# Kernel tuning notes

Hardware: AMD Instinct MI355X
Metric: run time of the kernel (lower is better)

The kernel has to match this reference:

```python
import jax, jax.numpy as jnp
import numpy as np
from jax import lax

D_MODEL = 200
N_LAYER = 12
NHEADS = 8
HEADDIM = 50
D_STATE = 64
D_INNER = 2 * D_MODEL            # 400
CONV_DIM = D_INNER + 2 * D_STATE  # 528 (ngroups=1)
D_IN_PROJ = 2 * D_INNER + 2 * D_STATE + NHEADS  # 936
D_CONV = 4
EPS = 1e-5


def rmsnorm(x, w):
    v = jnp.mean(jnp.square(x), axis=-1, keepdims=True)
    return x * lax.rsqrt(v + EPS) * w


def groupnorm(x, groups, g, b):
    B, C, H, W = x.shape
    xg = x.reshape(B, groups, C // groups, H, W)
    mu = jnp.mean(xg, axis=(2, 3, 4), keepdims=True)
    var = jnp.mean(jnp.square(xg - mu), axis=(2, 3, 4), keepdims=True)
    xn = ((xg - mu) * lax.rsqrt(var + EPS)).reshape(B, C, H, W)
    return xn * g[:, None, None] + b[:, None, None]


def patch_embed(x, pe_conv_w, proj_in_w, gn_g, gn_b, spec_w):
    b, c, l, d = x.shape
    # time path: 'b c l d' -> (b, 1, c*l, d), conv -> (b, 25, c*l, 8)
    time_x = x.reshape(b, 1, c * l, d)
    t = lax.conv_general_dilated(time_x, proj_in_w, (1, 25), ((0, 0), (24, 24)),
                                 dimension_numbers=('NCHW', 'OIHW', 'NCHW'))
    t = jax.nn.gelu(groupnorm(t, 5, gn_g, gn_b), approximate=False)
    time_emb = t.transpose(0, 2, 1, 3).reshape(b, c, l, D_MODEL)
    # freq path: rfft over patch dim, norm='forward'
    spec = jnp.abs(jnp.fft.rfft(x, axis=-1, norm='forward'))  # (b,c,l,101)
    spec_emb = jnp.einsum('bclf,df->bcld', spec, spec_w)
    patch = time_emb + spec_emb
    # depthwise 7x7 positional conv over (d, c, l)
    pos = lax.conv_general_dilated(patch.transpose(0, 3, 1, 2), pe_conv_w, (1, 1),
                                   ((3, 3), (3, 3)),
                                   dimension_numbers=('NCHW', 'OIHW', 'NCHW'),
                                   feature_group_count=D_MODEL)
    return patch + pos.transpose(0, 2, 3, 1)


def ssd_scan(xh, dt, B, C, A, D):
    # xh: (b,l,h,p)  dt: (b,l,h)  B,C: (b,l,n)  A,D: (h,)
    b, l, h, p = xh.shape

    def step(state, inp):
        x_t, dt_t, B_t, C_t = inp
        dA = jnp.exp(dt_t * A)  # (b,h)
        state = state * dA[:, :, None, None] + \
            (dt_t[:, :, None, None] * x_t[:, :, :, None]) * B_t[:, None, None, :]
        y = jnp.einsum('bhpn,bn->bhp', state, C_t)
        return state, y

    state0 = jnp.zeros((b, h, p, D_STATE), xh.dtype)
    _, ys = lax.scan(step, state0,
                     (xh.transpose(1, 0, 2, 3), dt.transpose(1, 0, 2),
                      B.transpose(1, 0, 2), C.transpose(1, 0, 2)))
    return ys.transpose(1, 0, 2, 3) + xh * D[None, None, :, None]


def mamba2(u, in_w, conv_w, conv_b, dt_bias, A_log, D, gn_w, out_w):
    b, l, _ = u.shape
    zxbcdt = u @ in_w.T  # (b,l,936)
    z = zxbcdt[..., :D_INNER]
    xBC = zxbcdt[..., D_INNER:D_INNER + CONV_DIM]
    dt = jax.nn.softplus(zxbcdt[..., D_INNER + CONV_DIM:] + dt_bias)  # (b,l,8)
    # causal depthwise conv1d, kernel 4
    xc = lax.conv_general_dilated(xBC.transpose(0, 2, 1), conv_w, (1,), ((D_CONV - 1, 0),),
                                  dimension_numbers=('NCH', 'OIH', 'NCH'),
                                  feature_group_count=CONV_DIM)
    xBC = jax.nn.silu((xc + conv_b[:, None]).transpose(0, 2, 1))
    x = xBC[..., :D_INNER].reshape(b, l, NHEADS, HEADDIM)
    Bm = xBC[..., D_INNER:D_INNER + D_STATE]
    Cm = xBC[..., D_INNER + D_STATE:]
    y = ssd_scan(x, dt, Bm, Cm, -jnp.exp(A_log), D).reshape(b, l, D_INNER)
    y = rmsnorm(y * jax.nn.silu(z), gn_w)  # RMSNormGated, norm_before_gate=False
    return y @ out_w.T


@jax.checkpoint
def layer(hidden, residual, norm_w, in_w, conv_w, conv_b, dt_bias, A_log, D, gn_w, out_w):
    residual = hidden + residual
    hidden = mamba2(rmsnorm(residual, norm_w), in_w, conv_w, conv_b, dt_bias, A_log, D, gn_w, out_w)
    return hidden, residual


def forward(x, pe_conv_w, proj_in_w, gn_g, gn_b, spec_w, norm_w, in_proj_w, conv_w, conv_b,
            dt_bias, A_log, D, gnorm_w, out_proj_w, norm_f_w, head_w, head_b):
    b, c, l, d = x.shape
    hidden = patch_embed(x, pe_conv_w, proj_in_w, gn_g, gn_b, spec_w).reshape(b, c * l, d)
    residual = jnp.zeros_like(hidden)
    for i in range(N_LAYER):
        hidden, residual = layer(hidden, residual, norm_w[i], in_proj_w[i], conv_w[i],
                                 conv_b[i], dt_bias[i], A_log[i], D[i], gnorm_w[i], out_proj_w[i])
    hidden = rmsnorm(hidden + residual, norm_f_w).reshape(b, c, l, d)
    return hidden @ head_w.T + head_b


def setup_inputs():
    key = jax.random.key(0)
    ks = jax.random.split(key, 12)
    B, CH, L, P = 16, 19, 30, 200

    def g(k, shape, scale):
        return jax.random.normal(k, shape, jnp.float32) * scale

    dt = jax.random.uniform(ks[8], (N_LAYER, NHEADS), jnp.float32, 1e-3, 0.1)
    return {
        'x': g(ks[0], (B, CH, L, P), 1.0),
        'pe_conv_w': g(ks[1], (D_MODEL, 1, 7, 7), 0.15),
        'proj_in_w': g(ks[2], (25, 1, 1, 49), 0.14),
        'gn_g': jnp.ones(25, jnp.float32),
        'gn_b': jnp.zeros(25, jnp.float32),
        'spec_w': g(ks[3], (D_MODEL, 101), 0.1),
        'norm_w': jnp.ones((N_LAYER, D_MODEL), jnp.float32),
        'in_proj_w': g(ks[4], (N_LAYER, D_IN_PROJ, D_MODEL), 0.07),
        'conv_w': g(ks[5], (N_LAYER, CONV_DIM, 1, D_CONV), 0.4),
        'conv_b': jnp.zeros((N_LAYER, CONV_DIM), jnp.float32),
        'dt_bias': jnp.log(jnp.expm1(dt)),
        'A_log': jnp.log(jax.random.uniform(ks[9], (N_LAYER, NHEADS), jnp.float32, 1.0, 16.0)),
        'D': jnp.ones((N_LAYER, NHEADS), jnp.float32),
        'gnorm_w': jnp.ones((N_LAYER, D_INNER), jnp.float32),
        'out_proj_w': g(ks[6], (N_LAYER, D_MODEL, D_INNER), 0.05),
        'norm_f_w': jnp.ones(D_MODEL, jnp.float32),
        'head_w': g(ks[7], (D_MODEL, D_MODEL), 0.07),
        'head_b': jnp.zeros(D_MODEL, jnp.float32),
    }


def reference(x, pe_conv_w, proj_in_w, gn_g, gn_b, spec_w, norm_w, in_proj_w, conv_w, conv_b,
              dt_bias, A_log, D, gnorm_w, out_proj_w, norm_f_w, head_w, head_b):
    return forward(x, pe_conv_w, proj_in_w, gn_g, gn_b, spec_w, norm_w, in_proj_w, conv_w,
                   conv_b, dt_bias, A_log, D, gnorm_w, out_proj_w, norm_f_w, head_w, head_b)
```

## Files before the change

kernel.cpp:

```cpp
#include <hip/hip_runtime.h>
#include <hip/hip_bf16.h>
#include <math.h>

#define D_MODEL   200
#define N_LAYER   12
#define NHEADS    8
#define HEADDIM   50
#define D_STATE   64
#define D_INNER   400
#define CONV_DIM  528
#define D_IN_PROJ 936
#define D_CONV    4
#define EPS       1e-5f

#define BATCH 16
#define CH    19
#define LLEN  30
#define SEQ   570
#define NTOK  9120
#define NFREQ 101

typedef __attribute__((ext_vector_type(8))) short s8v;
typedef __attribute__((ext_vector_type(4))) float f32x4;

// ... 416 lines not shown
        dtb[(size_t)m * NHEADS + h] = (raw > 20.f) ? raw : log1pf(expf(raw));
    }
}

__global__ __launch_bounds__(256) void dt_gemv_kernel(
    const float* __restrict__ u, const float* __restrict__ Win,
    const float* __restrict__ dt_bias, float* __restrict__ dtb, int layer)
{
    int tid = threadIdx.x;
    int tok = blockIdx.x * 4 + (tid >> 6);
    int head = (tid >> 3) & 7;
    int l8 = tid & 7;
    const float* ur = u + (size_t)tok * 200;
    const float* wr = Win + (size_t)layer * D_IN_PROJ * 200 + (size_t)(928 + head) * 200;
    float s = 0.f;
    for (int k = l8; k < 200; k += 8) s = fmaf(ur[k], wr[k], s);
    s += __shfl_xor(s, 1, 64);
    s += __shfl_xor(s, 2, 64);
    s += __shfl_xor(s, 4, 64);
    if (l8 == 0) {
        float raw = s + dt_bias[layer * NHEADS + head];
        dtb[(size_t)tok * NHEADS + head] = (raw > 20.f) ? raw : log1pf(expf(raw));
    }
}

__global__ __launch_bounds__(256) void dtconv2_kernel(
    const float* __restrict__ zxbcdt, const float* __restrict__ cw,
    const float* __restrict__ cb, float* __restrict__ xBC, int layer)
{
    int b = blockIdx.x, tt = blockIdx.y;
    int t0 = tt * 8;
    __shared__ float zs[11][528];
    const float* cwl = cw + (size_t)layer * CONV_DIM * 4;
    const float* cbl = cb + (size_t)layer * CONV_DIM;
    for (int i = threadIdx.x; i < 11 * 528; i += 256) {
        int r = i / 528, ch = i - r * 528;
        int t = t0 - 3 + r;
        zs[r][ch] = (t >= 0 && t < SEQ)
                        ? zxbcdt[(size_t)(b * SEQ + t) * D_IN_PROJ + D_INNER + ch] : 0.f;
    }
    __syncthreads();
    for (int o = threadIdx.x; o < 8 * 528; o += 256) {
        int tr = o / 528, ch = o - tr * 528;
        int t = t0 + tr;
        if (t >= SEQ) continue;
        float acc = cbl[ch];
#pragma unroll
        for (int k = 0; k < 4; k++)
            acc = fmaf(zs[tr + k][ch], cwl[ch * 4 + k], acc);
        xBC[(size_t)(b * SEQ + t) * CONV_DIM + ch] = acc / (1.f + expf(-acc));
    }
}

__global__ __launch_bounds__(512) void ssd_state3_kernel(
    const float* __restrict__ xBC, const float* __restrict__ dtb,
    const float* __restrict__ A_log, float* __restrict__ Sbuf,
    float* __restrict__ Pd, int layer, int lchunk, int nchunk)
{
    int b = blockIdx.x, c = blockIdx.y;
    int tid = threadIdx.x;
    int h = tid >> 6, p = tid & 63;
    float A = -expf(A_log[layer * NHEADS + h]);

    __shared__ __align__(16) float sh[2][2][536];
    int t0 = c * lchunk;
    int npairs = lchunk >> 1, rem = lchunk & 1;

    {
        if (tid < 264) {
            int wch = (tid >= 132) ? 1 : 0;
            int fidx = tid - wch * 132;
            int tq = t0 + wch;
            float4 v = ((const float4*)(xBC + (size_t)(b * SEQ + tq) * CONV_DIM))[fidx];
            *(float4*)&sh[0][wch][fidx * 4] = v;
        } else if (tid < 280) {
            int e = tid - 264, tok = e >> 3, hd = e & 7;
            sh[0][tok][528 + hd] = dtb[(size_t)(b * SEQ + t0 + tok) * NHEADS + hd];
        }
    }
    __syncthreads();

    float s[64];
#pragma unroll
    for (int n = 0; n < 64; n++) s[n] = 0.f;
    float pacc = 1.f;

    for (int i = 0; i < npairs; i++) {
        int t = t0 + 2 * i;
        int buf = i & 1, nb = buf ^ 1;
        bool pf = (2 * i + 2 < lchunk);
        float4 rx;
        float rdt = 0.f;
        int wch = 0, fidx = 0;
        if (pf) {
            if (tid < 264) {
                wch = (tid >= 132) ? 1 : 0;
                fidx = tid - wch * 132;
                int tq = t + 2 + wch; if (tq > SEQ - 1) tq = SEQ - 1;
                rx = ((const float4*)(xBC + (size_t)(b * SEQ + tq) * CONV_DIM))[fidx];
            } else if (tid < 280) {
                int e = tid - 264, tok = e >> 3, hd = e & 7;
                int tq = t + 2 + tok; if (tq > SEQ - 1) tq = SEQ - 1;
                rdt = dtb[(size_t)(b * SEQ + tq) * NHEADS + hd];
            }
        }
#pragma unroll
        for (int k = 0; k < 2; k++) {
            float dtv = sh[buf][k][528 + h];
            float xp  = (p < HEADDIM) ? sh[buf][k][h * HEADDIM + p] : 0.f;
            float dA = __expf(dtv * A);
            float u  = dtv * xp;
            pacc *= dA;
            const float4* B4 = (const float4*)&sh[buf][k][D_INNER];
#pragma unroll
            for (int n4 = 0; n4 < 16; n4++) {
                float4 bq = B4[n4];
                s[4 * n4 + 0] = fmaf(s[4 * n4 + 0], dA, u * bq.x);
                s[4 * n4 + 1] = fmaf(s[4 * n4 + 1], dA, u * bq.y);
                s[4 * n4 + 2] = fmaf(s[4 * n4 + 2], dA, u * bq.z);
                s[4 * n4 + 3] = fmaf(s[4 * n4 + 3], dA, u * bq.w);
            }
        }
        if (pf) {
            if (tid < 264) *(float4*)&sh[nb][wch][fidx * 4] = rx;
            else if (tid < 280) { int e = tid - 264; sh[nb][e >> 3][528 + (e & 7)] = rdt; }
        }
        __syncthreads();
    }

    if (rem) {
        int buf = npairs & 1;
        float dtv = sh[buf][0][528 + h];
        float xp  = (p < HEADDIM) ? sh[buf][0][h * HEADDIM + p] : 0.f;
        float dA = __expf(dtv * A);
        float u  = dtv * xp;
        pacc *= dA;
        const float4* B4 = (const float4*)&sh[buf][0][D_INNER];
#pragma unroll
        for (int n4 = 0; n4 < 16; n4++) {
            float4 bq = B4[n4];
            s[4 * n4 + 0] = fmaf(s[4 * n4 + 0], dA, u * bq.x);
            s[4 * n4 + 1] = fmaf(s[4 * n4 + 1], dA, u * bq.y);
            s[4 * n4 + 2] = fmaf(s[4 * n4 + 2], dA, u * bq.z);
            s[4 * n4 + 3] = fmaf(s[4 * n4 + 3], dA, u * bq.w);
        }
    }

    if (p < HEADDIM) {
        float* Sb = Sbuf + ((size_t)((b * NHEADS + h) * nchunk + c)) * (HEADDIM * 64)
                    + p * 64;
#pragma unroll
        for (int n4 = 0; n4 < 16; n4++)
            ((float4*)Sb)[n4] = make_float4(s[4 * n4], s[4 * n4 + 1],
                                            s[4 * n4 + 2], s[4 * n4 + 3]);
    }
    if (p == 0) Pd[(b * NHEADS + h) * nchunk + c] = pacc;
}

__global__ __launch_bounds__(512) void ssd_state_kernel(
    const float* __restrict__ xBC, const float* __restrict__ dtb,
    const float* __restrict__ A_log, float* __restrict__ Sbuf,
    float* __restrict__ Pd, int layer, int lchunk, int nchunk)
{
    int b = blockIdx.x, c = blockIdx.y;
    int tid = threadIdx.x;
    int h = tid >> 6, p = tid & 63;
    float A = -expf(A_log[layer * NHEADS + h]);

    __shared__ float sh[2][544];
    int t0 = c * lchunk, tend = t0 + lchunk;

    {
        const float* base = xBC + (size_t)(b * SEQ + t0) * CONV_DIM;
        sh[0][tid] = base[tid];
        if (tid < 24) {
            int e2 = 512 + tid;
            sh[0][e2] = (e2 < 528) ? base[e2]
                                   : dtb[(size_t)(b * SEQ + t0) * NHEADS + (e2 - 528)];
        }
    }
    __syncthreads();

    float s[64];
#pragma unroll
    for (int n = 0; n < 64; n++) s[n] = 0.f;
    float pacc = 1.f;

    for (int t = t0; t < tend; t++) {
        int cur = (t - t0) & 1, nxt = cur ^ 1;
        float pf0 = 0.f, pf1 = 0.f;
        if (t + 1 < tend) {
            const float* base = xBC + (size_t)(b * SEQ + t + 1) * CONV_DIM;
            pf0 = base[tid];
            if (tid < 24) {
                int e2 = 512 + tid;
                pf1 = (e2 < 528) ? base[e2]
                                 : dtb[(size_t)(b * SEQ + t + 1) * NHEADS + (e2 - 528)];
            }
        }
        float dtv = sh[cur][528 + h];
        float xp  = (p < HEADDIM) ? sh[cur][h * HEADDIM + p] : 0.f;
        float dA = __expf(dtv * A);
        float u  = dtv * xp;
        pacc *= dA;
        const float4* B4 = (const float4*)&sh[cur][D_INNER];
#pragma unroll
        for (int n4 = 0; n4 < 16; n4++) {
            float4 bq = B4[n4];
            s[4 * n4 + 0] = fmaf(s[4 * n4 + 0], dA, u * bq.x);
            s[4 * n4 + 1] = fmaf(s[4 * n4 + 1], dA, u * bq.y);
            s[4 * n4 + 2] = fmaf(s[4 * n4 + 2], dA, u * bq.z);
            s[4 * n4 + 3] = fmaf(s[4 * n4 + 3], dA, u * bq.w);
        }
        if (t + 1 < tend) {
            sh[nxt][tid] = pf0;
            if (tid < 24) sh[nxt][512 + tid] = pf1;
        }
        __syncthreads();
    }

    if (p < HEADDIM) {
        float* Sb = Sbuf + ((size_t)((b * NHEADS + h) * nchunk + c)) * (HEADDIM * 64)
                    + p * 64;
#pragma unroll
        for (int n4 = 0; n4 < 16; n4++)
            ((float4*)Sb)[n4] = make_float4(s[4 * n4], s[4 * n4 + 1],
                                            s[4 * n4 + 2], s[4 * n4 + 3]);
    }
    if (p == 0) Pd[(b * NHEADS + h) * nchunk + c] = pacc;
}

__global__ __launch_bounds__(256) void ssd_scan2b_kernel(
    float* __restrict__ Sbuf, const float* __restrict__ Pd, int nchunk)
{
    int bh = blockIdx.x;
    int e = blockIdx.y * 256 + threadIdx.x;
    if (e >= HEADDIM * 64) return;
    float* base = Sbuf + (size_t)bh * nchunk * (HEADDIM * 64) + e;
    const float* pd = Pd + bh * nchunk;
    float cur = 0.f;
    for (int c = 0; c < nchunk; c++) {
        float l = base[(size_t)c * (HEADDIM * 64)];
        base[(size_t)c * (HEADDIM * 64)] = cur;
        cur = fmaf(pd[c], cur, l);
    }
}

__global__ __launch_bounds__(512) void ssd_out_fused3_kernel(
    const float* __restrict__ xBC, const float* __restrict__ dtb,
    const float* __restrict__ zxbcdt, const float* __restrict__ A_log,
    const float* __restrict__ Dv, const float* __restrict__ Sbuf,
    const float* __restrict__ gw, short* __restrict__ ybf,
    int layer, int lchunk, int nchunk)
{
    int b = blockIdx.x, c = blockIdx.y;
    int tid = threadIdx.x;
    int h = tid >> 6, p = tid & 63;
    float A = -expf(A_log[layer * NHEADS + h]);
    float Dh = Dv[layer * NHEADS + h];
    float gval = (p < HEADDIM) ? gw[(size_t)layer * D_INNER + h * HEADDIM + p] : 0.f;

    __shared__ __align__(16) float sh[2][2][536];
    __shared__ __align__(16) float shz[2][2][400];
    __shared__ float red[2][2][8];
    int t0 = c * lchunk;
    int npairs = lchunk >> 1, rem = lchunk & 1;

    {
        if (tid < 264) {
            int wch = (tid >= 132) ? 1 : 0;
            int fidx = tid - wch * 132;
            int tq = t0 + wch;
            float4 v = ((const float4*)(xBC + (size_t)(b * SEQ + tq) * CONV_DIM))[fidx];
            *(float4*)&sh[0][wch][fidx * 4] = v;
        } else if (tid < 280) {
            int e = tid - 264, tok = e >> 3, hd = e & 7;
            sh[0][tok][528 + hd] = dtb[(size_t)(b * SEQ + t0 + tok) * NHEADS + hd];
        } else if (tid < 480) {
            int wch = (tid >= 380) ? 1 : 0;
            int fidx = tid - 280 - wch * 100;
            int tq = t0 + wch;
            float4 v = ((const float4*)(zxbcdt + (size_t)(b * SEQ + tq) * D_IN_PROJ))[fidx];
            *(float4*)&shz[0][wch][fidx * 4] = v;
        }
    }

    float s[64];
    if (p < HEADDIM) {
        const float* Sb = Sbuf + ((size_t)((b * NHEADS + h) * nchunk + c)) * (HEADDIM * 64)
                          + p * 64;
#pragma unroll
        for (int n4 = 0; n4 < 16; n4++) {
            float4 v = ((const float4*)Sb)[n4];
            s[4 * n4] = v.x; s[4 * n4 + 1] = v.y; s[4 * n4 + 2] = v.z; s[4 * n4 + 3] = v.w;
        }
    } else {
#pragma unroll
        for (int n = 0; n < 64; n++) s[n] = 0.f;
    }
    __syncthreads();

    for (int i = 0; i < npairs; i++) {
        int t = t0 + 2 * i;
        int buf = i & 1, nb = buf ^ 1;
        bool pf = (2 * i + 2 < lchunk);
        float4 rx, rz;
        float rdt = 0.f;
        int wch = 0, fidx = 0, zwch = 0, zfidx = 0;
        if (pf) {
            if (tid < 264) {
                wch = (tid >= 132) ? 1 : 0;
                fidx = tid - wch * 132;
                int tq = t + 2 + wch; if (tq > SEQ - 1) tq = SEQ - 1;
                rx = ((const float4*)(xBC + (size_t)(b * SEQ + tq) * CONV_DIM))[fidx];
            } else if (tid < 280) {
                int e = tid - 264, tok = e >> 3, hd = e & 7;
                int tq = t + 2 + tok; if (tq > SEQ - 1) tq = SEQ - 1;
                rdt = dtb[(size_t)(b * SEQ + tq) * NHEADS + hd];
            } else if (tid < 480) {
                zwch = (tid >= 380) ? 1 : 0;
                zfidx = tid - 280 - zwch * 100;
                int tq = t + 2 + zwch; if (tq > SEQ - 1) tq = SEQ - 1;
                rz = ((const float4*)(zxbcdt + (size_t)(b * SEQ + tq) * D_IN_PROJ))[zfidx];
            }
        }
        float g0 = 0.f, g1 = 0.f;
#pragma unroll
        for (int k = 0; k < 2; k++) {
            float dtv = sh[buf][k][528 + h];
            float xp  = (p < HEADDIM) ? sh[buf][k][h * HEADDIM + p] : 0.f;
            float dA = __expf(dtv * A);
            float u  = dtv * xp;
            const float4* B4 = (const float4*)&sh[buf][k][D_INNER];
            const float4* C4 = (const float4*)&sh[buf][k][D_INNER + D_STATE];
            float y0 = 0.f, y1 = 0.f, y2 = 0.f, y3 = 0.f;
#pragma unroll
            for (int n4 = 0; n4 < 16; n4++) {
                float4 bq = B4[n4];
                float4 cq = C4[n4];
                float t0v = fmaf(s[4 * n4 + 0], dA, u * bq.x);
                float t1v = fmaf(s[4 * n4 + 1], dA, u * bq.y);
                float t2v = fmaf(s[4 * n4 + 2], dA, u * bq.z);
                float t3v = fmaf(s[4 * n4 + 3], dA, u * bq.w);
                s[4 * n4 + 0] = t0v; s[4 * n4 + 1] = t1v;
                s[4 * n4 + 2] = t2v; s[4 * n4 + 3] = t3v;
                y0 = fmaf(t0v, cq.x, y0);
                y1 = fmaf(t1v, cq.y, y1);
                y2 = fmaf(t2v, cq.z, y2);
                y3 = fmaf(t3v, cq.w, y3);
            }
            if (p < HEADDIM) {
                float yv = fmaf(xp, Dh, (y0 + y1) + (y2 + y3));
                float zv = shz[buf][k][h * HEADDIM + p];
                float g = yv * (zv / (1.f + expf(-zv)));
                if (k == 0) g0 = g; else g1 = g;
            }
        }
        float gs0 = g0 * g0, gs1 = g1 * g1;
#pragma unroll
        for (int o = 32; o; o >>= 1) {
            gs0 += __shfl_xor(gs0, o, 64);
            gs1 += __shfl_xor(gs1, o, 64);
        }
        if (p == 0) { red[buf][0][h] = gs0; red[buf][1][h] = gs1; }
        if (pf) {
            if (tid < 264) *(float4*)&sh[nb][wch][fidx * 4] = rx;
            else if (tid < 280) { int e = tid - 264; sh[nb][e >> 3][528 + (e & 7)] = rdt; }
            else if (tid < 480) *(float4*)&shz[nb][zwch][zfidx * 4] = rz;
        }
        __syncthreads();
        float tot0 = (red[buf][0][0] + red[buf][0][1]) + (red[buf][0][2] + red[buf][0][3]) +
                     (red[buf][0][4] + red[buf][0][5]) + (red[buf][0][6] + red[buf][0][7]);
        float tot1 = (red[buf][1][0] + red[buf][1][1]) + (red[buf][1][2] + red[buf][1][3]) +
                     (red[buf][1][4] + red[buf][1][5]) + (red[buf][1][6] + red[buf][1][7]);
        float rstd0 = rsqrtf(tot0 * (1.f / D_INNER) + EPS);
        float rstd1 = rsqrtf(tot1 * (1.f / D_INNER) + EPS);
        size_t row0 = (size_t)(b * SEQ + t) * 416;
        size_t row1 = (size_t)(b * SEQ + t + 1) * 416;
        if (p < HEADDIM) {
            ybf[row0 + h * HEADDIM + p] = f2bf(g0 * rstd0 * gval);
            ybf[row1 + h * HEADDIM + p] = f2bf(g1 * rstd1 * gval);
        } else {
            int widx = h * 14 + (p - HEADDIM);
            if (widx < 16) {
                ybf[row0 + 400 + widx] = 0;
                ybf[row1 + 400 + widx] = 0;
            }
        }
    }

    if (rem) {
        int buf = npairs & 1;
        int t = t0 + lchunk - 1;
        float g0 = 0.f;
        {
            float dtv = sh[buf][0][528 + h];
            float xp  = (p < HEADDIM) ? sh[buf][0][h * HEADDIM + p] : 0.f;
            float dA = __expf(dtv * A);
            float u  = dtv * xp;
            const float4* B4 = (const float4*)&sh[buf][0][D_INNER];
            const float4* C4 = (const float4*)&sh[buf][0][D_INNER + D_STATE];
            float y0 = 0.f, y1 = 0.f, y2 = 0.f, y3 = 0.f;
#pragma unroll
            for (int n4 = 0; n4 < 16; n4++) {
                float4 bq = B4[n4];
                float4 cq = C4[n4];
                float t0v = fmaf(s[4 * n4 + 0], dA, u * bq.x);
                float t1v = fmaf(s[4 * n4 + 1], dA, u * bq.y);
                float t2v = fmaf(s[4 * n4 + 2], dA, u * bq.z);
                float t3v = fmaf(s[4 * n4 + 3], dA, u * bq.w);
                s[4 * n4 + 0] = t0v; s[4 * n4 + 1] = t1v;
                s[4 * n4 + 2] = t2v; s[4 * n4 + 3] = t3v;
                y0 = fmaf(t0v, cq.x, y0);
                y1 = fmaf(t1v, cq.y, y1);
                y2 = fmaf(t2v, cq.z, y2);
                y3 = fmaf(t3v, cq.w, y3);
            }
            if (p < HEADDIM) {
                float yv = fmaf(xp, Dh, (y0 + y1) + (y2 + y3));
                float zv = shz[buf][0][h * HEADDIM + p];
                g0 = yv * (zv / (1.f + expf(-zv)));
            }
        }
        float gs0 = g0 * g0;
#pragma unroll
        for (int o = 32; o; o >>= 1) gs0 += __shfl_xor(gs0, o, 64);
        if (p == 0) red[buf][0][h] = gs0;
        __syncthreads();
        float tot0 = (red[buf][0][0] + red[buf][0][1]) + (red[buf][0][2] + red[buf][0][3]) +
                     (red[buf][0][4] + red[buf][0][5]) + (red[buf][0][6] + red[buf][0][7]);
        float rstd0 = rsqrtf(tot0 * (1.f / D_INNER) + EPS);
        size_t row0 = (size_t)(b * SEQ + t) * 416;
        if (p < HEADDIM) {
            ybf[row0 + h * HEADDIM + p] = f2bf(g0 * rstd0 * gval);
        } else {
            int widx = h * 14 + (p - HEADDIM);
            if (widx < 16) ybf[row0 + 400 + widx] = 0;
        }
    }
}

__global__ __launch_bounds__(512) void ssd_out_kernel(
    const float* __restrict__ xBC, const float* __restrict__ dtb,
    const float* __restrict__ A_log, const float* __restrict__ Dv,
    const float* __restrict__ Sbuf, float* __restrict__ y,
    int layer, int lchunk, int nchunk)
{
    int b = blockIdx.x, c = blockIdx.y;
    int tid = threadIdx.x;
    int h = tid >> 6, p = tid & 63;
    float A = -expf(A_log[layer * NHEADS + h]);
    float Dh = Dv[layer * NHEADS + h];

    __shared__ float sh[2][544];
    int t0 = c * lchunk, tend = t0 + lchunk;

    {
        const float* base = xBC + (size_t)(b * SEQ + t0) * CONV_DIM;
        sh[0][tid] = base[tid];
        if (tid < 24) {
            int e2 = 512 + tid;
            sh[0][e2] = (e2 < 528) ? base[e2]
                                   : dtb[(size_t)(b * SEQ + t0) * NHEADS + (e2 - 528)];
        }
    }

    float s[64];
    if (p < HEADDIM) {
        const float* Sb = Sbuf + ((size_t)((b * NHEADS + h) * nchunk + c)) * (HEADDIM * 64)
                          + p * 64;
#pragma unroll
        for (int n4 = 0; n4 < 16; n4++) {
            float4 v = ((const float4*)Sb)[n4];
            s[4 * n4] = v.x; s[4 * n4 + 1] = v.y; s[4 * n4 + 2] = v.z; s[4 * n4 + 3] = v.w;
        }
    } else {
#pragma unroll
        for (int n = 0; n < 64; n++) s[n] = 0.f;
    }
    __syncthreads();

    for (int t = t0; t < tend; t++) {
        int cur = (t - t0) & 1, nxt = cur ^ 1;
        float pf0 = 0.f, pf1 = 0.f;
        if (t + 1 < tend) {
            const float* base = xBC + (size_t)(b * SEQ + t + 1) * CONV_DIM;
            pf0 = base[tid];
            if (tid < 24) {
                int e2 = 512 + tid;
                pf1 = (e2 < 528) ? base[e2]
// ... 45 lines not shown
    float* yr = y + (size_t)m * D_INNER;
    const float* gwl = gw + (size_t)layer * D_INNER;
    float ss = 0.f;
    for (int k = threadIdx.x; k < D_INNER; k += 256) {
        float zv = z[k];
        float sz = zv / (1.f + expf(-zv));
        float g = yr[k] * sz;
        buf[k] = g;
        ss = fmaf(g, g, ss);
    }
    int lane = threadIdx.x & 63, w = threadIdx.x >> 6;
#pragma unroll
    for (int o = 32; o; o >>= 1) ss += __shfl_xor(ss, o, 64);
    if (lane == 0) red[w] = ss;
    __syncthreads();
    float tot = red[0] + red[1] + red[2] + red[3];
    float rstd = rsqrtf(tot * (1.f / D_INNER) + EPS);
    for (int k = threadIdx.x; k < 416; k += 256) {
        if (k < D_INNER) {
            float v = buf[k] * rstd * gwl[k];
            yr[k] = v;
            if (ybf) ybf[(size_t)m * 416 + k] = f2bf(v);
        } else if (ybf) {
            ybf[(size_t)m * 416 + k] = 0;
        }
    }
}

extern "C" void kernel_launch(void* const* d_in, const int* in_sizes, int n_in,
                              void* d_out, int out_size, void* d_ws, size_t ws_size,
                              hipStream_t stream)
{
    const float* x         = (const float*)d_in[0];
    const float* pe_conv_w = (const float*)d_in[1];
    const float* proj_in_w = (const float*)d_in[2];
    const float* gn_g      = (const float*)d_in[3];
    const float* gn_b      = (const float*)d_in[4];
    const float* spec_w    = (const float*)d_in[5];
    const float* norm_w    = (const float*)d_in[6];
    const float* in_proj_w = (const float*)d_in[7];
    const float* conv_w    = (const float*)d_in[8];
    const float* conv_b    = (const float*)d_in[9];
    const float* dt_bias   = (const float*)d_in[10];
    const float* A_log     = (const float*)d_in[11];
    const float* Dv        = (const float*)d_in[12];
    const float* gnorm_w   = (const float*)d_in[13];
    const float* out_proj_w= (const float*)d_in[14];
    const float* norm_f_w  = (const float*)d_in[15];
    const float* head_w    = (const float*)d_in[16];
    const float* head_b    = (const float*)d_in[17];
    float* out = (float*)d_out;
    float* ws  = (float*)d_ws;

    const size_t needA = 27929344ull * sizeof(float);
    int fast = (ws_size >= needA) ? 1 : 0;

    int nchunk, lchunk;
    float *residual = ws, *hidden = ws + 1824000;
    float *zxbcdt, *xBC, *dtb, *Sbuf, *Pd;
    float *ubuf = nullptr, *ybuf = nullptr;
    short *w_in_bf = nullptr, *w_out_bf = nullptr, *w_head_bf = nullptr,
          *w_spec_bf = nullptr, *csmat_bf = nullptr, *x_bf = nullptr,
          *ubuf_bf = nullptr, *ybuf_bf = nullptr, *magb_bf = nullptr;

    if (fast) {
        nchunk = 15; lchunk = 38;
        zxbcdt = ws + 3648000;
        xBC    = ws + 12184320;
        dtb    = ws + 16999680;
        Sbuf   = ws + 17072640;
        Pd     = ws + 23216640;
        short* pool = (short*)(ws + 23218560);
        w_in_bf   = pool;
        w_out_bf  = pool + 2515968;
        w_head_bf = pool + 3514368;
        w_spec_bf = pool + 3559168;
        ubuf_bf   = pool + 3584768;
        ybuf_bf   = pool + 5627648;
        csmat_bf  = (short*)(Sbuf + 4000000);
        x_bf      = (short*)(Sbuf + 4100000);
        magb_bf   = (short*)(Sbuf + 5200000);
    } else {
        nchunk = 6; lchunk = 95;
        ubuf   = ws + 3648000;
        zxbcdt = ws + 5472000;
        xBC    = ws + 14008320;
        dtb    = ws + 18823680;
        ybuf   = ws + 18896640;
        Sbuf   = ws + 1824000;
        Pd     = ws + 5470000;
    }

    float* traw  = fast ? Sbuf : ybuf;
    float* patch = zxbcdt;
    float* csout = fast ? (Sbuf + 2000000) : (xBC + 50000);
    float* csmat = xBC;
    float* magb  = fast ? nullptr : (xBC + 2000000);
    float* stats = dtb;

    if (fast) {
        cast_pad_kernel<<<(12 * 936 * 224 + 255) / 256, 256, 0, stream>>>(
            in_proj_w, w_in_bf, 12 * 936, 200, 224);
        cast_pad_kernel<<<(12 * 200 * 416 + 255) / 256, 256, 0, stream>>>(
            out_proj_w, w_out_bf, 12 * 200, 400, 416);
        cast_pad_kernel<<<(200 * 224 + 255) / 256, 256, 0, stream>>>(
            head_w, w_head_bf, 200, 200, 224);
        cast_pad_kernel<<<(200 * 128 + 255) / 256, 256, 0, stream>>>(
            spec_w, w_spec_bf, 200, 101, 128);
        cast_pad_kernel<<<(9120 * 224 + 255) / 256, 256, 0, stream>>>(
            x, x_bf, 9120, 200, 224);
        dft_init_bf_kernel<<<(202 * 224 + 255) / 256, 256, 0, stream>>>(csmat_bf);
    } else {
        dft_init_kernel<<<(202 * 200 + 255) / 256, 256, 0, stream>>>(csmat);
    }

    time_conv_kernel<<<NTOK, 256, 0, stream>>>(x, proj_in_w, traw);
    gn_stats_kernel<<<80, 256, 0, stream>>>(traw, stats);
    gn_gelu_kernel<<<(NTOK * 200 + 255) / 256, 256, 0, stream>>>(traw, stats, gn_g, gn_b, patch);
    if (fast) {
        gemm_bf16<<<dim3(2, 72), 256, 0, stream>>>(x_bf, csmat_bf, nullptr, csout,
                                                   NTOK, 202, 224, 0);
        mag_bf_kernel<<<(NTOK * 128 + 255) / 256, 256, 0, stream>>>(csout, magb_bf);
        gemm_bf16<<<dim3(2, 72), 256, 0, stream>>>(magb_bf, w_spec_bf, nullptr, patch,
                                                   NTOK, 200, 128, 1);
    } else {
        gemm_nt<<<dim3(2, 72), 256, 0, stream>>>(x, csmat, nullptr, csout, NTOK, 202, 200, 0);
        mag_kernel<<<(NTOK * NFREQ + 255) / 256, 256, 0, stream>>>(csout, magb);
        gemm_nt<<<dim3(2, 72), 256, 0, stream>>>(magb, spec_w, nullptr, patch,
                                                 NTOK, 200, NFREQ, 1);
    }
    pe_conv3_kernel<<<dim3(16, 13, 5), 256, 0, stream>>>(patch, pe_conv_w, hidden);

    for (int i = 0; i < N_LAYER; i++) {
        if (fast) {
            norm_dt_kernel<<<NTOK, 256, 0, stream>>>(hidden, residual, norm_w + i * 200,
                                                     ubuf_bf, in_proj_w, dt_bias, dtb,
                                                     i, (i == 0) ? 1 : 0);
            gemm_bf16<<<dim3(8, 72), 256, 0, stream>>>(
                ubuf_bf, w_in_bf + (size_t)i * 936 * 224, nullptr, zxbcdt,
                NTOK, D_IN_PROJ, 224, 0);
        } else {
            add_rmsnorm_kernel<<<NTOK, 64, 0, stream>>>(hidden, residual, norm_w + i * 200,
                                                        ubuf, nullptr, (i == 0) ? 1 : 0);
            dt_gemv_kernel<<<NTOK / 4, 256, 0, stream>>>(ubuf, in_proj_w, dt_bias, dtb, i);
            gemm_nt<<<dim3(8, 72), 256, 0, stream>>>(
                ubuf, in_proj_w + (size_t)i * D_IN_PROJ * 200, nullptr, zxbcdt,
                NTOK, D_IN_PROJ, 200, 0);
        }
        dtconv2_kernel<<<dim3(16, 72), 256, 0, stream>>>(zxbcdt, conv_w, conv_b, xBC, i);
        {
            dim3 g(BATCH, nchunk);
            if (fast) {
                ssd_state3_kernel<<<g, 512, 0, stream>>>(xBC, dtb, A_log, Sbuf, Pd,
                                                         i, lchunk, nchunk);
                ssd_scan2b_kernel<<<dim3(BATCH * NHEADS, 13), 256, 0, stream>>>(Sbuf, Pd, nchunk);
                ssd_out_fused3_kernel<<<g, 512, 0, stream>>>(
                    xBC, dtb, zxbcdt, A_log, Dv, Sbuf, gnorm_w, ybuf_bf, i, lchunk, nchunk);
                gemm_bf16<<<dim3(2, 72), 256, 0, stream>>>(
                    ybuf_bf, w_out_bf + (size_t)i * 200 * 416, nullptr, hidden,
                    NTOK, 200, 416, 0);
            } else {
                ssd_state_kernel<<<g, 512, 0, stream>>>(xBC, dtb, A_log, Sbuf, Pd,
                                                        i, lchunk, nchunk);
                ssd_scan2b_kernel<<<dim3(BATCH * NHEADS, 13), 256, 0, stream>>>(Sbuf, Pd, nchunk);
                ssd_out_kernel<<<g, 512, 0, stream>>>(xBC, dtb, A_log, Dv, Sbuf, ybuf,
                                                      i, lchunk, nchunk);
                gate_norm_kernel<<<NTOK, 256, 0, stream>>>(ybuf, zxbcdt, gnorm_w, nullptr, i);
                gemm_nt<<<dim3(2, 72), 256, 0, stream>>>(
                    ybuf, out_proj_w + (size_t)i * 200 * D_INNER, nullptr, hidden,
                    NTOK, 200, D_INNER, 0);
            }
        }
    }

    add_rmsnorm_kernel<<<NTOK, 64, 0, stream>>>(hidden, residual, norm_f_w,
                                                fast ? nullptr : ubuf,
                                                fast ? ubuf_bf : nullptr, 0);
    if (fast) {
        gemm_bf16<<<dim3(2, 72), 256, 0, stream>>>(ubuf_bf, w_head_bf, head_b, out,
                                                   NTOK, 200, 224, 0);
    } else {
        gemm_nt<<<dim3(2, 72), 256, 0, stream>>>(ubuf, head_w, head_b, out,
                                                 NTOK, 200, 200, 0);
    }
}
```

Baseline: 2.542 ms.

## Compute local chunk outputs in state pass; apply inter-chunk correction separately

The first scan kernel now produces each token's within-chunk output (including the D skip term) and the running decay product, in addition to the chunk-final states. It uses a triple-buffered shared-memory prefetch that loads two token pairs ahead. A new correction kernel adds the carried-in state contribution, scaled by the prefix decay, as a C·S0 dot product, then applies the gate and RMS norm. This removes the second full recurrence over B that the old output kernel redid. In exchange it writes and reads an extra fp32 y buffer and prefix array in a larger workspace. The odd-length remainder path was dropped, so the code assumes lchunk is even (38 here).

```diff
diff --git a/kernel.cpp b/kernel.cpp
--- a/kernel.cpp
+++ b/kernel.cpp
@@ -492,30 +492,33 @@
     }
 }
 
-__global__ __launch_bounds__(512) void ssd_state3_kernel(
+__global__ __launch_bounds__(512) void ssd_scanA_kernel(
     const float* __restrict__ xBC, const float* __restrict__ dtb,
-    const float* __restrict__ A_log, float* __restrict__ Sbuf,
-    float* __restrict__ Pd, int layer, int lchunk, int nchunk)
+    const float* __restrict__ A_log, const float* __restrict__ Dv,
+    float* __restrict__ ylocal, float* __restrict__ Pref,
+    float* __restrict__ Sbuf, float* __restrict__ Pd,
+    int layer, int lchunk, int nchunk)
 {
     int b = blockIdx.x, c = blockIdx.y;
     int tid = threadIdx.x;
     int h = tid >> 6, p = tid & 63;
     float A = -expf(A_log[layer * NHEADS + h]);
-
-    __shared__ __align__(16) float sh[2][2][536];
+    float Dh = Dv[layer * NHEADS + h];
+
+    __shared__ __align__(16) float sh[3][2][536];
     int t0 = c * lchunk;
-    int npairs = lchunk >> 1, rem = lchunk & 1;
-
-    {
+    int npairs = lchunk >> 1;
+
+    for (int j = 0; j < 2 && j < npairs; j++) {
         if (tid < 264) {
             int wch = (tid >= 132) ? 1 : 0;
             int fidx = tid - wch * 132;
-            int tq = t0 + wch;
+            int tq = t0 + 2 * j + wch;
             float4 v = ((const float4*)(xBC + (size_t)(b * SEQ + tq) * CONV_DIM))[fidx];
-            *(float4*)&sh[0][wch][fidx * 4] = v;
+            *(float4*)&sh[j][wch][fidx * 4] = v;
         } else if (tid < 280) {
             int e = tid - 264, tok = e >> 3, hd = e & 7;
-            sh[0][tok][528 + hd] = dtb[(size_t)(b * SEQ + t0 + tok) * NHEADS + hd];
+            sh[j][tok][528 + hd] = dtb[(size_t)(b * SEQ + t0 + 2 * j + tok) * NHEADS + hd];
         }
     }
     __syncthreads();
@@ -527,8 +530,9 @@
 
     for (int i = 0; i < npairs; i++) {
         int t = t0 + 2 * i;
-        int buf = i & 1, nb = buf ^ 1;
-        bool pf = (2 * i + 2 < lchunk);
+        int buf = i % 3;
+        int nb = (i + 2) % 3;
+        bool pf = (i + 2 < npairs);
         float4 rx;
         float rdt = 0.f;
         int wch = 0, fidx = 0;
@@ -536,12 +540,11 @@
             if (tid < 264) {
                 wch = (tid >= 132) ? 1 : 0;
                 fidx = tid - wch * 132;
-                int tq = t + 2 + wch; if (tq > SEQ - 1) tq = SEQ - 1;
+                int tq = t + 4 + wch;
                 rx = ((const float4*)(xBC + (size_t)(b * SEQ + tq) * CONV_DIM))[fidx];
             } else if (tid < 280) {
                 int e = tid - 264, tok = e >> 3, hd = e & 7;
-                int tq = t + 2 + tok; if (tq > SEQ - 1) tq = SEQ - 1;
-                rdt = dtb[(size_t)(b * SEQ + tq) * NHEADS + hd];
+                rdt = dtb[(size_t)(b * SEQ + t + 4 + tok) * NHEADS + hd];
             }
         }
 #pragma unroll
@@ -551,226 +554,6 @@
             float dA = __expf(dtv * A);
             float u  = dtv * xp;
             pacc *= dA;
-            const float4* B4 = (const float4*)&sh[buf][k][D_INNER];
-#pragma unroll
-            for (int n4 = 0; n4 < 16; n4++) {
-                float4 bq = B4[n4];
-                s[4 * n4 + 0] = fmaf(s[4 * n4 + 0], dA, u * bq.x);
-                s[4 * n4 + 1] = fmaf(s[4 * n4 + 1], dA, u * bq.y);
-                s[4 * n4 + 2] = fmaf(s[4 * n4 + 2], dA, u * bq.z);
-                s[4 * n4 + 3] = fmaf(s[4 * n4 + 3], dA, u * bq.w);
-            }
-        }
-        if (pf) {
-            if (tid < 264) *(float4*)&sh[nb][wch][fidx * 4] = rx;
-            else if (tid < 280) { int e = tid - 264; sh[nb][e >> 3][528 + (e & 7)] = rdt; }
-        }
-        __syncthreads();
-    }
-
-    if (rem) {
-        int buf = npairs & 1;
-        float dtv = sh[buf][0][528 + h];
-        float xp  = (p < HEADDIM) ? sh[buf][0][h * HEADDIM + p] : 0.f;
-        float dA = __expf(dtv * A);
-        float u  = dtv * xp;
-        pacc *= dA;
-        const float4* B4 = (const float4*)&sh[buf][0][D_INNER];
-#pragma unroll
-        for (int n4 = 0; n4 < 16; n4++) {
-            float4 bq = B4[n4];
-            s[4 * n4 + 0] = fmaf(s[4 * n4 + 0], dA, u * bq.x);
-            s[4 * n4 + 1] = fmaf(s[4 * n4 + 1], dA, u * bq.y);
-            s[4 * n4 + 2] = fmaf(s[4 * n4 + 2], dA, u * bq.z);
-            s[4 * n4 + 3] = fmaf(s[4 * n4 + 3], dA, u * bq.w);
-        }
-    }
-
-    if (p < HEADDIM) {
-        float* Sb = Sbuf + ((size_t)((b * NHEADS + h) * nchunk + c)) * (HEADDIM * 64)
-                    + p * 64;
-#pragma unroll
-        for (int n4 = 0; n4 < 16; n4++)
-            ((float4*)Sb)[n4] = make_float4(s[4 * n4], s[4 * n4 + 1],
-                                            s[4 * n4 + 2], s[4 * n4 + 3]);
-    }
-    if (p == 0) Pd[(b * NHEADS + h) * nchunk + c] = pacc;
-}
-
-__global__ __launch_bounds__(512) void ssd_state_kernel(
-    const float* __restrict__ xBC, const float* __restrict__ dtb,
-    const float* __restrict__ A_log, float* __restrict__ Sbuf,
-    float* __restrict__ Pd, int layer, int lchunk, int nchunk)
-{
-    int b = blockIdx.x, c = blockIdx.y;
-    int tid = threadIdx.x;
-    int h = tid >> 6, p = tid & 63;
-    float A = -expf(A_log[layer * NHEADS + h]);
-
-    __shared__ float sh[2][544];
-    int t0 = c * lchunk, tend = t0 + lchunk;
-
-    {
-        const float* base = xBC + (size_t)(b * SEQ + t0) * CONV_DIM;
-        sh[0][tid] = base[tid];
-        if (tid < 24) {
-            int e2 = 512 + tid;
-            sh[0][e2] = (e2 < 528) ? base[e2]
-                                   : dtb[(size_t)(b * SEQ + t0) * NHEADS + (e2 - 528)];
-        }
-    }
-    __syncthreads();
-
-    float s[64];
-#pragma unroll
-    for (int n = 0; n < 64; n++) s[n] = 0.f;
-    float pacc = 1.f;
-
-    for (int t = t0; t < tend; t++) {
-        int cur = (t - t0) & 1, nxt = cur ^ 1;
-        float pf0 = 0.f, pf1 = 0.f;
-        if (t + 1 < tend) {
-            const float* base = xBC + (size_t)(b * SEQ + t + 1) * CONV_DIM;
-            pf0 = base[tid];
-            if (tid < 24) {
-                int e2 = 512 + tid;
-                pf1 = (e2 < 528) ? base[e2]
-                                 : dtb[(size_t)(b * SEQ + t + 1) * NHEADS + (e2 - 528)];
-            }
-        }
-        float dtv = sh[cur][528 + h];
-        float xp  = (p < HEADDIM) ? sh[cur][h * HEADDIM + p] : 0.f;
-        float dA = __expf(dtv * A);
-        float u  = dtv * xp;
-        pacc *= dA;
-        const float4* B4 = (const float4*)&sh[cur][D_INNER];
-#pragma unroll
-        for (int n4 = 0; n4 < 16; n4++) {
-            float4 bq = B4[n4];
-            s[4 * n4 + 0] = fmaf(s[4 * n4 + 0], dA, u * bq.x);
-            s[4 * n4 + 1] = fmaf(s[4 * n4 + 1], dA, u * bq.y);
-            s[4 * n4 + 2] = fmaf(s[4 * n4 + 2], dA, u * bq.z);
-            s[4 * n4 + 3] = fmaf(s[4 * n4 + 3], dA, u * bq.w);
-        }
-        if (t + 1 < tend) {
-            sh[nxt][tid] = pf0;
-            if (tid < 24) sh[nxt][512 + tid] = pf1;
-        }
-        __syncthreads();
-    }
-
-    if (p < HEADDIM) {
-        float* Sb = Sbuf + ((size_t)((b * NHEADS + h) * nchunk + c)) * (HEADDIM * 64)
-                    + p * 64;
-#pragma unroll
-        for (int n4 = 0; n4 < 16; n4++)
-            ((float4*)Sb)[n4] = make_float4(s[4 * n4], s[4 * n4 + 1],
-                                            s[4 * n4 + 2], s[4 * n4 + 3]);
-    }
-    if (p == 0) Pd[(b * NHEADS + h) * nchunk + c] = pacc;
-}
-
-__global__ __launch_bounds__(256) void ssd_scan2b_kernel(
-    float* __restrict__ Sbuf, const float* __restrict__ Pd, int nchunk)
-{
-    int bh = blockIdx.x;
-    int e = blockIdx.y * 256 + threadIdx.x;
-    if (e >= HEADDIM * 64) return;
-    float* base = Sbuf + (size_t)bh * nchunk * (HEADDIM * 64) + e;
-    const float* pd = Pd + bh * nchunk;
-    float cur = 0.f;
-    for (int c = 0; c < nchunk; c++) {
-        float l = base[(size_t)c * (HEADDIM * 64)];
-        base[(size_t)c * (HEADDIM * 64)] = cur;
-        cur = fmaf(pd[c], cur, l);
-    }
-}
-
-__global__ __launch_bounds__(512) void ssd_out_fused3_kernel(
-    const float* __restrict__ xBC, const float* __restrict__ dtb,
-    const float* __restrict__ zxbcdt, const float* __restrict__ A_log,
-    const float* __restrict__ Dv, const float* __restrict__ Sbuf,
-    const float* __restrict__ gw, short* __restrict__ ybf,
-    int layer, int lchunk, int nchunk)
-{
-    int b = blockIdx.x, c = blockIdx.y;
-    int tid = threadIdx.x;
-    int h = tid >> 6, p = tid & 63;
-    float A = -expf(A_log[layer * NHEADS + h]);
-    float Dh = Dv[layer * NHEADS + h];
-    float gval = (p < HEADDIM) ? gw[(size_t)layer * D_INNER + h * HEADDIM + p] : 0.f;
-
-    __shared__ __align__(16) float sh[2][2][536];
-    __shared__ __align__(16) float shz[2][2][400];
-    __shared__ float red[2][2][8];
-    int t0 = c * lchunk;
-    int npairs = lchunk >> 1, rem = lchunk & 1;
-
-    {
-        if (tid < 264) {
-            int wch = (tid >= 132) ? 1 : 0;
-            int fidx = tid - wch * 132;
-            int tq = t0 + wch;
-            float4 v = ((const float4*)(xBC + (size_t)(b * SEQ + tq) * CONV_DIM))[fidx];
-            *(float4*)&sh[0][wch][fidx * 4] = v;
-        } else if (tid < 280) {
-            int e = tid - 264, tok = e >> 3, hd = e & 7;
-            sh[0][tok][528 + hd] = dtb[(size_t)(b * SEQ + t0 + tok) * NHEADS + hd];
-        } else if (tid < 480) {
-            int wch = (tid >= 380) ? 1 : 0;
-            int fidx = tid - 280 - wch * 100;
-            int tq = t0 + wch;
-            float4 v = ((const float4*)(zxbcdt + (size_t)(b * SEQ + tq) * D_IN_PROJ))[fidx];
-            *(float4*)&shz[0][wch][fidx * 4] = v;
-        }
-    }
-
-    float s[64];
-    if (p < HEADDIM) {
-        const float* Sb = Sbuf + ((size_t)((b * NHEADS + h) * nchunk + c)) * (HEADDIM * 64)
-                          + p * 64;
-#pragma unroll
-        for (int n4 = 0; n4 < 16; n4++) {
-            float4 v = ((const float4*)Sb)[n4];
-            s[4 * n4] = v.x; s[4 * n4 + 1] = v.y; s[4 * n4 + 2] = v.z; s[4 * n4 + 3] = v.w;
-        }
-    } else {
-#pragma unroll
-        for (int n = 0; n < 64; n++) s[n] = 0.f;
-    }
-    __syncthreads();
-
-    for (int i = 0; i < npairs; i++) {
-        int t = t0 + 2 * i;
-        int buf = i & 1, nb = buf ^ 1;
-        bool pf = (2 * i + 2 < lchunk);
-        float4 rx, rz;
-        float rdt = 0.f;
-        int wch = 0, fidx = 0, zwch = 0, zfidx = 0;
-        if (pf) {
-            if (tid < 264) {
-                wch = (tid >= 132) ? 1 : 0;
-                fidx = tid - wch * 132;
-                int tq = t + 2 + wch; if (tq > SEQ - 1) tq = SEQ - 1;
-                rx = ((const float4*)(xBC + (size_t)(b * SEQ + tq) * CONV_DIM))[fidx];
-            } else if (tid < 280) {
-                int e = tid - 264, tok = e >> 3, hd = e & 7;
-                int tq = t + 2 + tok; if (tq > SEQ - 1) tq = SEQ - 1;
-                rdt = dtb[(size_t)(b * SEQ + tq) * NHEADS + hd];
-            } else if (tid < 480) {
-                zwch = (tid >= 380) ? 1 : 0;
-                zfidx = tid - 280 - zwch * 100;
-                int tq = t + 2 + zwch; if (tq > SEQ - 1) tq = SEQ - 1;
-                rz = ((const float4*)(zxbcdt + (size_t)(b * SEQ + tq) * D_IN_PROJ))[zfidx];
-            }
-        }
-        float g0 = 0.f, g1 = 0.f;
-#pragma unroll
-        for (int k = 0; k < 2; k++) {
-            float dtv = sh[buf][k][528 + h];
-            float xp  = (p < HEADDIM) ? sh[buf][k][h * HEADDIM + p] : 0.f;
-            float dA = __expf(dtv * A);
-            float u  = dtv * xp;
             const float4* B4 = (const float4*)&sh[buf][k][D_INNER];
             const float4* C4 = (const float4*)&sh[buf][k][D_INNER + D_STATE];
             float y0 = 0.f, y1 = 0.f, y2 = 0.f, y3 = 0.f;
@@ -789,12 +572,206 @@
                 y2 = fmaf(t2v, cq.z, y2);
                 y3 = fmaf(t3v, cq.w, y3);
             }
-            if (p < HEADDIM) {
-                float yv = fmaf(xp, Dh, (y0 + y1) + (y2 + y3));
-                float zv = shz[buf][k][h * HEADDIM + p];
-                float g = yv * (zv / (1.f + expf(-zv)));
-                if (k == 0) g0 = g; else g1 = g;
-            }
+            if (p < HEADDIM)
+                ylocal[(size_t)(b * SEQ + t + k) * D_INNER + h * HEADDIM + p] =
+                    fmaf(xp, Dh, (y0 + y1) + (y2 + y3));
+            if (p == 0)
+                Pref[(size_t)(b * SEQ + t + k) * NHEADS + h] = pacc;
+        }
+        if (pf) {
+            if (tid < 264) *(float4*)&sh[nb][wch][fidx * 4] = rx;
+            else if (tid < 280) { int e = tid - 264; sh[nb][e >> 3][528 + (e & 7)] = rdt; }
+        }
+        __syncthreads();
+    }
+
+    if (p < HEADDIM) {
+        float* Sb = Sbuf + ((size_t)((b * NHEADS + h) * nchunk + c)) * (HEADDIM * 64)
+                    + p * 64;
+#pragma unroll
+        for (int n4 = 0; n4 < 16; n4++)
+            ((float4*)Sb)[n4] = make_float4(s[4 * n4], s[4 * n4 + 1],
+                                            s[4 * n4 + 2], s[4 * n4 + 3]);
+    }
+    if (p == 0) Pd[(b * NHEADS + h) * nchunk + c] = pacc;
+}
+
+__global__ __launch_bounds__(512) void ssd_state_kernel(
+    const float* __restrict__ xBC, const float* __restrict__ dtb,
+    const float* __restrict__ A_log, float* __restrict__ Sbuf,
+    float* __restrict__ Pd, int layer, int lchunk, int nchunk)
+{
+    int b = blockIdx.x, c = blockIdx.y;
+    int tid = threadIdx.x;
+    int h = tid >> 6, p = tid & 63;
+    float A = -expf(A_log[layer * NHEADS + h]);
+
+    __shared__ float sh[2][544];
+    int t0 = c * lchunk, tend = t0 + lchunk;
+
+    {
+        const float* base = xBC + (size_t)(b * SEQ + t0) * CONV_DIM;
+        sh[0][tid] = base[tid];
+        if (tid < 24) {
+            int e2 = 512 + tid;
+            sh[0][e2] = (e2 < 528) ? base[e2]
+                                   : dtb[(size_t)(b * SEQ + t0) * NHEADS + (e2 - 528)];
+        }
+    }
+    __syncthreads();
+
+    float s[64];
+#pragma unroll
+    for (int n = 0; n < 64; n++) s[n] = 0.f;
+    float pacc = 1.f;
+
+    for (int t = t0; t < tend; t++) {
+        int cur = (t - t0) & 1, nxt = cur ^ 1;
+        float pf0 = 0.f, pf1 = 0.f;
+        if (t + 1 < tend) {
+            const float* base = xBC + (size_t)(b * SEQ + t + 1) * CONV_DIM;
+            pf0 = base[tid];
+            if (tid < 24) {
+                int e2 = 512 + tid;
+                pf1 = (e2 < 528) ? base[e2]
+                                 : dtb[(size_t)(b * SEQ + t + 1) * NHEADS + (e2 - 528)];
+            }
+        }
+        float dtv = sh[cur][528 + h];
+        float xp  = (p < HEADDIM) ? sh[cur][h * HEADDIM + p] : 0.f;
+        float dA = __expf(dtv * A);
+        float u  = dtv * xp;
+        pacc *= dA;
+        const float4* B4 = (const float4*)&sh[cur][D_INNER];
+#pragma unroll
+        for (int n4 = 0; n4 < 16; n4++) {
+            float4 bq = B4[n4];
+            s[4 * n4 + 0] = fmaf(s[4 * n4 + 0], dA, u * bq.x);
+            s[4 * n4 + 1] = fmaf(s[4 * n4 + 1], dA, u * bq.y);
+            s[4 * n4 + 2] = fmaf(s[4 * n4 + 2], dA, u * bq.z);
+            s[4 * n4 + 3] = fmaf(s[4 * n4 + 3], dA, u * bq.w);
+        }
+        if (t + 1 < tend) {
+            sh[nxt][tid] = pf0;
+            if (tid < 24) sh[nxt][512 + tid] = pf1;
+        }
+        __syncthreads();
+    }
+
+    if (p < HEADDIM) {
+        float* Sb = Sbuf + ((size_t)((b * NHEADS + h) * nchunk + c)) * (HEADDIM * 64)
+                    + p * 64;
+#pragma unroll
+        for (int n4 = 0; n4 < 16; n4++)
+            ((float4*)Sb)[n4] = make_float4(s[4 * n4], s[4 * n4 + 1],
+                                            s[4 * n4 + 2], s[4 * n4 + 3]);
+    }
+    if (p == 0) Pd[(b * NHEADS + h) * nchunk + c] = pacc;
+}
+
+__global__ __launch_bounds__(256) void ssd_scan2b_kernel(
+    float* __restrict__ Sbuf, const float* __restrict__ Pd, int nchunk)
+{
+    int bh = blockIdx.x;
+    int e = blockIdx.y * 256 + threadIdx.x;
+    if (e >= HEADDIM * 64) return;
+    float* base = Sbuf + (size_t)bh * nchunk * (HEADDIM * 64) + e;
+    const float* pd = Pd + bh * nchunk;
+    float cur = 0.f;
+    for (int c = 0; c < nchunk; c++) {
+        float l = base[(size_t)c * (HEADDIM * 64)];
+        base[(size_t)c * (HEADDIM * 64)] = cur;
+        cur = fmaf(pd[c], cur, l);
+    }
+}
+
+__global__ __launch_bounds__(512) void ssd_corr_kernel(
+    const float* __restrict__ xBC, const float* __restrict__ zxbcdt,
+    const float* __restrict__ ylocal, const float* __restrict__ Pref,
+    const float* __restrict__ Sbuf, const float* __restrict__ gw,
+    short* __restrict__ ybf, int layer, int lchunk, int nchunk)
+{
+    int b = blockIdx.x, c = blockIdx.y;
+    int tid = threadIdx.x;
+    int h = tid >> 6, p = tid & 63;
+    float gval = (p < HEADDIM) ? gw[(size_t)layer * D_INNER + h * HEADDIM + p] : 0.f;
+
+    __shared__ __align__(16) float Cst[2][2][64];
+    __shared__ float pfs[2][2][8];
+    __shared__ float red[2][2][8];
+    int t0 = c * lchunk;
+    int npairs = lchunk >> 1;
+
+    float s0[64];
+    if (p < HEADDIM) {
+        const float* Sb = Sbuf + ((size_t)((b * NHEADS + h) * nchunk + c)) * (HEADDIM * 64)
+                          + p * 64;
+#pragma unroll
+        for (int n4 = 0; n4 < 16; n4++) {
+            float4 v = ((const float4*)Sb)[n4];
+            s0[4 * n4] = v.x; s0[4 * n4 + 1] = v.y;
+            s0[4 * n4 + 2] = v.z; s0[4 * n4 + 3] = v.w;
+        }
+    } else {
+#pragma unroll
+        for (int n = 0; n < 64; n++) s0[n] = 0.f;
+    }
+
+    int col = h * HEADDIM + ((p < HEADDIM) ? p : 0);
+
+    if (tid < 128) {
+        int k = tid >> 6, n = tid & 63;
+        Cst[0][k][n] = xBC[(size_t)(b * SEQ + t0 + k) * CONV_DIM + D_INNER + D_STATE + n];
+    } else if (tid < 144) {
+        int e = tid - 128, k = e >> 3, hd = e & 7;
+        pfs[0][k][hd] = Pref[(size_t)(b * SEQ + t0 + k) * NHEADS + hd];
+    }
+    float ylr[2], zvr[2];
+#pragma unroll
+    for (int k = 0; k < 2; k++) {
+        ylr[k] = ylocal[(size_t)(b * SEQ + t0 + k) * D_INNER + col];
+        zvr[k] = zxbcdt[(size_t)(b * SEQ + t0 + k) * D_IN_PROJ + col];
+    }
+    __syncthreads();
+
+    for (int i = 0; i < npairs; i++) {
+        int t = t0 + 2 * i;
+        int buf = i & 1, nb = buf ^ 1;
+        bool pf = (i + 1 < npairs);
+        float rc = 0.f, rpf = 0.f, yln[2], zvn[2];
+        if (pf) {
+            if (tid < 128) {
+                int k = tid >> 6, n = tid & 63;
+                rc = xBC[(size_t)(b * SEQ + t + 2 + k) * CONV_DIM + D_INNER + D_STATE + n];
+            } else if (tid < 144) {
+                int e = tid - 128, k = e >> 3, hd = e & 7;
+                rpf = Pref[(size_t)(b * SEQ + t + 2 + k) * NHEADS + hd];
+            }
+#pragma unroll
+            for (int k = 0; k < 2; k++) {
+                yln[k] = ylocal[(size_t)(b * SEQ + t + 2 + k) * D_INNER + col];
+                zvn[k] = zxbcdt[(size_t)(b * SEQ + t + 2 + k) * D_IN_PROJ + col];
+            }
+        }
+        float g0 = 0.f, g1 = 0.f;
+#pragma unroll
+        for (int k = 0; k < 2; k++) {
+            const float4* C4 = (const float4*)&Cst[buf][k][0];
+            float c0 = 0.f, c1 = 0.f, c2 = 0.f, c3 = 0.f;
+#pragma unroll
+            for (int n4 = 0; n4 < 16; n4++) {
+                float4 cq = C4[n4];
+                c0 = fmaf(s0[4 * n4 + 0], cq.x, c0);
+                c1 = fmaf(s0[4 * n4 + 1], cq.y, c1);
+                c2 = fmaf(s0[4 * n4 + 2], cq.z, c2);
+                c3 = fmaf(s0[4 * n4 + 3], cq.w, c3);
+            }
+            float corr = (c0 + c1) + (c2 + c3);
+            float yv = fmaf(pfs[buf][k][h], corr, ylr[k]);
+            float zv = zvr[k];
+            float gg = yv * (zv / (1.f + expf(-zv)));
+            gg = (p < HEADDIM) ? gg : 0.f;
+            if (k == 0) g0 = gg; else g1 = gg;
         }
         float gs0 = g0 * g0, gs1 = g1 * g1;
 #pragma unroll
@@ -804,9 +781,10 @@
         }
         if (p == 0) { red[buf][0][h] = gs0; red[buf][1][h] = gs1; }
         if (pf) {
-            if (tid < 264) *(float4*)&sh[nb][wch][fidx * 4] = rx;
-            else if (tid < 280) { int e = tid - 264; sh[nb][e >> 3][528 + (e & 7)] = rdt; }
-            else if (tid < 480) *(float4*)&shz[nb][zwch][zfidx * 4] = rz;
+            if (tid < 128) { int k = tid >> 6, n = tid & 63; Cst[nb][k][n] = rc; }
+            else if (tid < 144) { int e = tid - 128; pfs[nb][e >> 3][e & 7] = rpf; }
+            ylr[0] = yln[0]; ylr[1] = yln[1];
+            zvr[0] = zvn[0]; zvr[1] = zvn[1];
         }
         __syncthreads();
         float tot0 = (red[buf][0][0] + red[buf][0][1]) + (red[buf][0][2] + red[buf][0][3]) +
@@ -826,56 +804,6 @@
                 ybf[row0 + 400 + widx] = 0;
                 ybf[row1 + 400 + widx] = 0;
             }
-        }
-    }
-
-    if (rem) {
-        int buf = npairs & 1;
-        int t = t0 + lchunk - 1;
-        float g0 = 0.f;
-        {
-            float dtv = sh[buf][0][528 + h];
-            float xp  = (p < HEADDIM) ? sh[buf][0][h * HEADDIM + p] : 0.f;
-            float dA = __expf(dtv * A);
-            float u  = dtv * xp;
-            const float4* B4 = (const float4*)&sh[buf][0][D_INNER];
-            const float4* C4 = (const float4*)&sh[buf][0][D_INNER + D_STATE];
-            float y0 = 0.f, y1 = 0.f, y2 = 0.f, y3 = 0.f;
-#pragma unroll
-            for (int n4 = 0; n4 < 16; n4++) {
-                float4 bq = B4[n4];
-                float4 cq = C4[n4];
-                float t0v = fmaf(s[4 * n4 + 0], dA, u * bq.x);
-                float t1v = fmaf(s[4 * n4 + 1], dA, u * bq.y);
-                float t2v = fmaf(s[4 * n4 + 2], dA, u * bq.z);
-                float t3v = fmaf(s[4 * n4 + 3], dA, u * bq.w);
-                s[4 * n4 + 0] = t0v; s[4 * n4 + 1] = t1v;
-                s[4 * n4 + 2] = t2v; s[4 * n4 + 3] = t3v;
-                y0 = fmaf(t0v, cq.x, y0);
-                y1 = fmaf(t1v, cq.y, y1);
-                y2 = fmaf(t2v, cq.z, y2);
-                y3 = fmaf(t3v, cq.w, y3);
-            }
-            if (p < HEADDIM) {
-                float yv = fmaf(xp, Dh, (y0 + y1) + (y2 + y3));
-                float zv = shz[buf][0][h * HEADDIM + p];
-                g0 = yv * (zv / (1.f + expf(-zv)));
-            }
-        }
-        float gs0 = g0 * g0;
-#pragma unroll
-        for (int o = 32; o; o >>= 1) gs0 += __shfl_xor(gs0, o, 64);
-        if (p == 0) red[buf][0][h] = gs0;
-        __syncthreads();
-        float tot0 = (red[buf][0][0] + red[buf][0][1]) + (red[buf][0][2] + red[buf][0][3]) +
-                     (red[buf][0][4] + red[buf][0][5]) + (red[buf][0][6] + red[buf][0][7]);
-        float rstd0 = rsqrtf(tot0 * (1.f / D_INNER) + EPS);
-        size_t row0 = (size_t)(b * SEQ + t) * 416;
-        if (p < HEADDIM) {
-            ybf[row0 + h * HEADDIM + p] = f2bf(g0 * rstd0 * gval);
-        } else {
-            int widx = h * 14 + (p - HEADDIM);
-            if (widx < 16) ybf[row0 + 400 + widx] = 0;
         }
     }
 }
@@ -1027,13 +955,13 @@
     float* out = (float*)d_out;
     float* ws  = (float*)d_ws;
 
-    const size_t needA = 27929344ull * sizeof(float);
+    const size_t needA = 31650304ull * sizeof(float);
     int fast = (ws_size >= needA) ? 1 : 0;
 
     int nchunk, lchunk;
     float *residual = ws, *hidden = ws + 1824000;
     float *zxbcdt, *xBC, *dtb, *Sbuf, *Pd;
-    float *ubuf = nullptr, *ybuf = nullptr;
+    float *ubuf = nullptr, *ybuf = nullptr, *ybuf_s = nullptr, *Pref = nullptr;
     short *w_in_bf = nullptr, *w_out_bf = nullptr, *w_head_bf = nullptr,
           *w_spec_bf = nullptr, *csmat_bf = nullptr, *x_bf = nullptr,
           *ubuf_bf = nullptr, *ybuf_bf = nullptr, *magb_bf = nullptr;
@@ -1052,6 +980,8 @@
         w_spec_bf = pool + 3559168;
         ubuf_bf   = pool + 3584768;
         ybuf_bf   = pool + 5627648;
+        ybuf_s    = ws + 27929344;
+        Pref      = ws + 31577344;
         csmat_bf  = (short*)(Sbuf + 4000000);
         x_bf      = (short*)(Sbuf + 4100000);
         magb_bf   = (short*)(Sbuf + 5200000);
@@ -1126,11 +1056,12 @@
         {
             dim3 g(BATCH, nchunk);
             if (fast) {
-                ssd_state3_kernel<<<g, 512, 0, stream>>>(xBC, dtb, A_log, Sbuf, Pd,
-                                                         i, lchunk, nchunk);
+                ssd_scanA_kernel<<<g, 512, 0, stream>>>(xBC, dtb, A_log, Dv,
+                                                        ybuf_s, Pref, Sbuf, Pd,
+                                                        i, lchunk, nchunk);
                 ssd_scan2b_kernel<<<dim3(BATCH * NHEADS, 13), 256, 0, stream>>>(Sbuf, Pd, nchunk);
-                ssd_out_fused3_kernel<<<g, 512, 0, stream>>>(
-                    xBC, dtb, zxbcdt, A_log, Dv, Sbuf, gnorm_w, ybuf_bf, i, lchunk, nchunk);
+                ssd_corr_kernel<<<g, 512, 0, stream>>>(
+                    xBC, zxbcdt, ybuf_s, Pref, Sbuf, gnorm_w, ybuf_bf, i, lchunk, nchunk);
                 gemm_bf16<<<dim3(2, 72), 256, 0, stream>>>(
                     ybuf_bf, w_out_bf + (size_t)i * 200 * 416, nullptr, hidden,
                     NTOK, 200, 416, 0);
```

Result: no change. 2.565 ms (+0.9%).
